# Performance work log

Hardware: AMD Instinct MI355X
Metric: run time of the kernel (lower is better)

## Reference

```python
import jax, jax.numpy as jnp
import numpy as np

D_IN = 2048
D_OUT = 2048
NUM_HEADS = 16
HEAD_DIM = D_OUT // NUM_HEADS  # 128
LATENT_DIM = 256
B, S = 2, 2048


def setup_inputs() -> dict:
    key = jax.random.key(0)
    ks = jax.random.split(key, 7)
    scale = 0.02
    return {
        "x": jax.random.normal(ks[0], (B, S, D_IN), dtype=jnp.float32),
        "W_query": jax.random.normal(ks[1], (D_IN, D_OUT), dtype=jnp.float32) * scale,
        "W_DKV": jax.random.normal(ks[2], (D_IN, LATENT_DIM), dtype=jnp.float32) * scale,
        "W_UKV": jax.random.normal(ks[3], (LATENT_DIM, 2 * D_OUT), dtype=jnp.float32) * scale,
        "W_out": jax.random.normal(ks[4], (D_OUT, D_IN), dtype=jnp.float32) * scale,
        "b_out": jax.random.normal(ks[5], (D_IN,), dtype=jnp.float32) * scale,
        "offset": 0,
    }


def reference(x, W_query, W_DKV, W_UKV, W_out, b_out, offset):
    Bq, Sq, _ = x.shape
    # projections
    q = x @ W_query                      # [B, S, d_out]
    latent = x @ W_DKV                   # [B, S, latent_dim]
    kv = latent @ W_UKV                  # [B, S, 2*d_out]
    k, v = jnp.split(kv, 2, axis=-1)     # each [B, S, d_out]

    def to_heads(t):
        return t.reshape(Bq, Sq, NUM_HEADS, HEAD_DIM).transpose(0, 2, 1, 3)  # [B, H, S, hd]

    qh, kh, vh = to_heads(q), to_heads(k), to_heads(v)

    scores = jnp.einsum("bhqd,bhkd->bhqk", qh, kh)  # [B, H, S, S]
    causal = jnp.tril(jnp.ones((Sq, Sq), dtype=bool))  # True = keep (kv_cache=None -> Sq==Skv)
    # faithful to original: masked_fill(-inf) BEFORE the rsqrt(head_dim) scaling
    scores = jnp.where(causal, scores, -jnp.inf)
    inv_sqrt_d = jax.lax.rsqrt(jnp.asarray(HEAD_DIM, dtype=scores.dtype))
    attn = jax.nn.softmax(scores * inv_sqrt_d, axis=-1)  # dropout p=0 -> identity

    ctx = jnp.einsum("bhqk,bhkd->bhqd", attn, vh)        # [B, H, S, hd]
    ctx = ctx.transpose(0, 2, 1, 3).reshape(Bq, Sq, D_OUT)
    return ctx @ W_out + b_out           # [B, S, d_in]
```

## Files before the change

kernel.cpp:

```cpp
#include <hip/hip_runtime.h>
#include <hip/hip_bf16.h>

typedef short bf16x8 __attribute__((ext_vector_type(8)));
typedef float f32x4 __attribute__((ext_vector_type(4)));
typedef float f32x16 __attribute__((ext_vector_type(16)));
typedef unsigned int u32x4 __attribute__((ext_vector_type(4)));
typedef unsigned short u16;
typedef unsigned short u16x4 __attribute__((ext_vector_type(4)));
typedef unsigned short u16x8 __attribute__((ext_vector_type(8)));

constexpr int D_IN = 2048, D_OUT = 2048, NH = 16, HD = 128, LAT = 256;
constexpr int Bb = 2, Ss = 2048, Mtot = Bb * Ss;

constexpr float QSCALE = 0.08838834764831845f * 1.4426950408889634f;
constexpr float NEG_BIG = -3.0e38f;

__device__ __forceinline__ u16 f2bf(float f) {
  unsigned u = __float_as_uint(f);
  unsigned r = ((u >> 16) & 1u) + 0x7fffu;
  return (u16)((u + r) >> 16);
}

__device__ __forceinline__ float bf2f(u16 v) {
  return __uint_as_float((unsigned)v << 16);
}

__device__ __forceinline__ float fexp2(float x) {
#if __has_builtin(__builtin_amdgcn_exp2f)
  return __builtin_amdgcn_exp2f(x);
#else
  return exp2f(x);
#endif
}

__device__ __forceinline__ unsigned cvtpk(float lo, float hi) {
  unsigned r;
  asm("v_cvt_pk_bf16_f32 %0, %1, %2" : "=v"(r) : "v"(lo), "v"(hi));
  return r;
}

__device__ __forceinline__ void swap32(unsigned& a, unsigned& b) {
  asm volatile("v_permlane32_swap_b32 %0, %1" : "+v"(a), "+v"(b));
}

__device__ __forceinline__ void gload_lds16(const u16* g, u16* l) {
  __builtin_amdgcn_global_load_lds((const __attribute__((address_space(1))) void*)g,
                                   (__attribute__((address_space(3))) void*)l, 16, 0, 0);
}

__global__ void k_cvt_all(const float* __restrict__ x, u16* __restrict__ xb,
                          const float* __restrict__ w0, u16* __restrict__ o0,
                          const float* __restrict__ w1, u16* __restrict__ o1,
                          const float* __restrict__ w2, u16* __restrict__ o2,
                          const float* __restrict__ w3, u16* __restrict__ o3) {
  int id = blockIdx.x;
  const int tx = threadIdx.x, ty = threadIdx.y;
  if (id < 8192) {
    const int i = id * 1024 + (ty * 32 + tx) * 4;
    float4 v = *reinterpret_cast<const float4*>(x + i);
    ushort4 o;
    o.x = f2bf(v.x); o.y = f2bf(v.y); o.z = f2bf(v.z); o.w = f2bf(v.w);
    *reinterpret_cast<ushort4*>(xb + i) = o;
    return;
  }
  id -= 8192;
  __shared__ float t[32][33];
  const float* in;
  u16* out;
  int K, N, bx, by;
  if (id < 4096)      { in = w0; out = o0; K = 2048; N = 2048; bx = (id & 63) * 32; by = (id >> 6) * 32; }
  else if (id < 4608) { id -= 4096; in = w1; out = o1; K = 2048; N = 256;  bx = (id & 7) * 32;  by = (id >> 3) * 32; }
  else if (id < 5632) { id -= 4608; in = w2; out = o2; K = 256;  N = 4096; bx = (id & 127) * 32; by = (id >> 7) * 32; }
  else                { id -= 5632; in = w3; out = o3; K = 2048; N = 2048; bx = (id & 63) * 32; by = (id >> 6) * 32; }
#pragma unroll
  for (int j = 0; j < 32; j += 8)
    t[ty + j][tx] = in[(size_t)(by + ty + j) * N + bx + tx];
  __syncthreads();
#pragma unroll
  for (int j = 0; j < 32; j += 8)
    out[(size_t)(bx + ty + j) * K + by + tx] = f2bf(t[tx][ty + j]);
}

template <int OUT_MODE>
__global__ __launch_bounds__(256) void k_gemm(const u16* __restrict__ A,
                                              const u16* __restrict__ Bt,
                                              void* __restrict__ Cp,
                                              void* __restrict__ Cp2,
                                              const float* __restrict__ bias,
                                              float scale, int M, int N, int K) {
  constexpr int BK = 64;
  __shared__ __align__(16) u16 As[128 * BK];
  __shared__ __align__(16) u16 Bs[128 * BK];
  const int nwg = gridDim.x;
  int bid = blockIdx.x;
  bid = (bid & 7) * (nwg >> 3) + (bid >> 3);
  const int nbx = N >> 7;
  const int bx = bid % nbx, by = bid / nbx;
  const int row0 = by << 7, col0 = bx << 7;
  const int tid = threadIdx.x;
  const int wave = tid >> 6, lane = tid & 63;
  const int wr = (wave >> 1) * 64, wc = (wave & 1) * 64;
  const int lr = lane & 15, lg = lane >> 4;

  f32x4 acc[4][4];
#pragma unroll
  for (int m = 0; m < 4; ++m)
#pragma unroll
    for (int n = 0; n < 4; ++n) acc[m][n] = (f32x4)0.0f;

  const int srow = wave * 32 + (lane >> 3);
  const int scol = ((lane & 7) ^ (lane >> 3)) * 8;
  const u16* gA = A + (size_t)(row0 + srow) * K + scol;
  const u16* gB = Bt + (size_t)(col0 + srow) * K + scol;
  const size_t rstep = (size_t)8 * K;
  u16* lA = &As[(wave * 32) * BK];
  u16* lB = &Bs[(wave * 32) * BK];

  const int rsw = (lr & 7) * 8;

  for (int k0 = 0; k0 < K; k0 += BK) {
#pragma unroll
    for (int c = 0; c < 4; ++c) {
      gload_lds16(gA + c * rstep + k0, lA + c * 8 * BK);
      gload_lds16(gB + c * rstep + k0, lB + c * 8 * BK);
    }
    __syncthreads();
#pragma unroll
    for (int sub = 0; sub < 2; ++sub) {
      const int co = (sub * 32 + lg * 8) ^ rsw;
      bf16x8 af[4], bfr[4];
#pragma unroll
      for (int m = 0; m < 4; ++m)
        af[m] = *reinterpret_cast<const bf16x8*>(&As[(wr + m * 16 + lr) * BK + co]);
#pragma unroll
      for (int n = 0; n < 4; ++n)
        bfr[n] = *reinterpret_cast<const bf16x8*>(&Bs[(wc + n * 16 + lr) * BK + co]);
#pragma unroll
      for (int m = 0; m < 4; ++m)
#pragma unroll
        for (int n = 0; n < 4; ++n)
          acc[m][n] = __builtin_amdgcn_mfma_f32_16x16x32_bf16(af[m], bfr[n], acc[m][n], 0, 0, 0);
    }
    __syncthreads();
  }

#pragma unroll
  for (int m = 0; m < 4; ++m) {
    const int r = row0 + wr + m * 16 + lg * 4;
#pragma unroll
    for (int n = 0; n < 4; ++n) {
      const int c = col0 + wc + n * 16 + lr;
#pragma unroll
      for (int i = 0; i < 4; ++i) {
        float v = acc[m][n][i];
        if (OUT_MODE == 0)
          ((u16*)Cp)[(size_t)(r + i) * N + c] = f2bf(v);
        else if (OUT_MODE == 1)
          ((float*)Cp)[(size_t)(r + i) * N + c] = v + bias[c];
        else {
          if (c < 2048)
            ((u16*)Cp)[(size_t)(r + i) * 2048 + c] = f2bf(v * scale);
          else
            ((u16*)Cp2)[(size_t)(r + i) * 256 + (c - 2048)] = f2bf(v);
        }
      }
    }
  }
}

__device__ __constant__ const signed char S_qb[16] = {7,0, 7,0, 6,0, 6,1, 5,0, 5,2, 4,0, 4,3};
__device__ __constant__ const signed char S_k0[16] = {0,0, 9,0, 0,0, 9,0, 0,0, 9,0, 0,0, 9,0};
__device__ __constant__ const signed char S_k1[16] = {9,0, 16,2, 9,0, 14,4, 9,0, 12,6, 9,0, 10,8};
__device__ __constant__ const signed char S_pm[16] = {0,0, 1,-1, 0,0, 1,-1, 0,0, 1,-1, 0,0, 1,-1};

__global__ __launch_bounds__(512) void k_attn(const u16* __restrict__ Q,
                                              const u16* __restrict__ KV,
                                              u16* __restrict__ O,
                                              u16* __restrict__ o_part,
                                              float* __restrict__ lbuf) {
  __shared__ __align__(16) u16 Ks[128 * 128];
  __shared__ __align__(16) u16 Vt[128 * 128];
  const int job = blockIdx.x >> 5, bh = blockIdx.x & 31;
  const int b = bh >> 4, h = bh & 15;
  const u16* Qb = Q + (size_t)b * Ss * D_OUT + h * HD;
  const u16* Kb = KV + (size_t)b * Ss * (2 * D_OUT) + h * HD;
  const u16* Vb = Kb + D_OUT;
  u16* Ob = O + (size_t)b * Ss * D_OUT + h * HD;

  const int tid = threadIdx.x, wave = tid >> 6, lane = tid & 63;
  const int lo = lane & 31, hi = lane >> 5;

  const int sr = tid >> 2, sc = tid & 3;
  const int vk = (tid & 31) * 4, vd = (tid >> 5) * 8;
  const size_t kvstep = (size_t)128 * 2 * D_OUT;
  const int ksw = (sr & 7) ^ (((sr >> 3) & 3) << 1);
  const int krd = ((lo & 7) * 8) ^ (((lo >> 3) & 3) << 4);

  for (int seg = 0; seg < 2; ++seg) {
    const int kt1 = S_k1[job * 2 + seg];
    if (kt1 == 0) break;
    const int qb = S_qb[job * 2 + seg];
    const int kt0 = S_k0[job * 2 + seg];
    const int pm = S_pm[job * 2 + seg];
    const int q0w = qb * 256 + wave * 32;

    bf16x8 qf[8];
    {
      const u16* qsrc = Qb + (size_t)(q0w + lo) * D_OUT + hi * 8;
#pragma unroll
      for (int ds = 0; ds < 8; ++ds)
        qf[ds] = *reinterpret_cast<const bf16x8*>(qsrc + ds * 16);
    }

    f32x16 ctx[4];
#pragma unroll
    for (int dt = 0; dt < 4; ++dt) ctx[dt] = (f32x16)0.0f;
    float lrow = 0.0f;

    const u16* kg = Kb + (size_t)kt0 * kvstep + (size_t)sr * (2 * D_OUT) + sc * 8;
    const u16* vg = Vb + (size_t)kt0 * kvstep + (size_t)vk * (2 * D_OUT) + vd;

    int4 kreg[4];
    u16x8 vreg[4];
#pragma unroll
    for (int c = 0; c < 4; ++c) {
      kreg[c] = *reinterpret_cast<const int4*>(kg + c * 32);
      vreg[c] = *reinterpret_cast<const u16x8*>(vg + (size_t)c * (2 * D_OUT));
    }

    for (int kt = kt0; kt < kt1; ++kt) {
#pragma unroll
      for (int c = 0; c < 4; ++c)
        *reinterpret_cast<int4*>(&Ks[sr * 128 + (((sc + 4 * c) ^ ksw) * 8)]) = kreg[c];
#pragma unroll
      for (int jj = 0; jj < 8; ++jj) {
        const int vcol = (vk ^ (jj * 8)) ^ ((((vd + jj) >> 3) & 3) << 4);
        u16x4 pk = {vreg[0][jj], vreg[1][jj], vreg[2][jj], vreg[3][jj]};
        *reinterpret_cast<u16x4*>(&Vt[(vd + jj) * 128 + vcol]) = pk;
      }
      if (kt + 1 < kt1) {
        const u16* kn = kg + (size_t)(kt + 1 - kt0) * kvstep;
        const u16* vn = vg + (size_t)(kt + 1 - kt0) * kvstep;
#pragma unroll
        for (int c = 0; c < 4; ++c) {
          kreg[c] = *reinterpret_cast<const int4*>(kn + c * 32);
          vreg[c] = *reinterpret_cast<const u16x8*>(vn + (size_t)c * (2 * D_OUT));
        }
      }
      __syncthreads();

#pragma unroll
      for (int sub = 0; sub < 2; ++sub) {
        const int kbs = kt * 128 + sub * 64;
        if (kbs <= q0w + 31) {
          f32x16 s0 = (f32x16)0.0f, s1 = (f32x16)0.0f;
          __builtin_amdgcn_s_setprio(1);
#pragma unroll
          for (int ds = 0; ds < 8; ++ds) {
            const int off = (16 * ds + 8 * hi) ^ krd;
            bf16x8 a0 = *reinterpret_cast<const bf16x8*>(&Ks[(sub * 64 + lo) * 128 + off]);
            bf16x8 a1 = *reinterpret_cast<const bf16x8*>(&Ks[(sub * 64 + 32 + lo) * 128 + off]);
            s0 = __builtin_amdgcn_mfma_f32_32x32x16_bf16(a0, qf[ds], s0, 0, 0, 0);
            s1 = __builtin_amdgcn_mfma_f32_32x32x16_bf16(a1, qf[ds], s1, 0, 0, 0);
          }
          __builtin_amdgcn_s_setprio(0);

          if (kbs + 63 > q0w) {
            const int qg = q0w + lo;
#pragma unroll
            for (int r = 0; r < 16; ++r) {
              const int koff = kbs + (r & 3) + 8 * (r >> 2) + 4 * hi;
              if (koff > qg) s0[r] = NEG_BIG;
              if (koff + 32 > qg) s1[r] = NEG_BIG;
            }
          }

#pragma unroll
          for (int r = 0; r < 16; ++r) s0[r] = fexp2(s0[r]);
#pragma unroll
          for (int r = 0; r < 16; ++r) s1[r] = fexp2(s1[r]);

          bf16x8 pa[4];
#pragma unroll
          for (int g = 0; g < 2; ++g) {
            const f32x16& sg = g ? s1 : s0;
#pragma unroll
            for (int half = 0; half < 2; ++half) {
              const int rb = half * 8;
              unsigned w0 = cvtpk(sg[rb + 0], sg[rb + 1]);
              unsigned w2 = cvtpk(sg[rb + 4], sg[rb + 5]);
              unsigned w1 = cvtpk(sg[rb + 2], sg[rb + 3]);
              unsigned w3 = cvtpk(sg[rb + 6], sg[rb + 7]);
              swap32(w0, w2);
              swap32(w1, w3);
              u32x4 fr = {w0, w1, w2, w3};
              pa[2 * g + half] = __builtin_bit_cast(bf16x8, fr);
            }
          }

          __builtin_amdgcn_s_setprio(1);
#pragma unroll
          for (int dt = 0; dt < 4; ++dt) {
            const int vrow = 32 * dt + lo;
#pragma unroll
            for (int ks = 0; ks < 4; ++ks) {
              const int off = sub * 64 + ((16 * ks + 8 * hi) ^ krd);
              bf16x8 bv = *reinterpret_cast<const bf16x8*>(&Vt[vrow * 128 + off]);
              ctx[dt] = __builtin_amdgcn_mfma_f32_32x32x16_bf16(pa[ks], bv, ctx[dt], 0, 0, 0);
            }
          }
          __builtin_amdgcn_s_setprio(0);

          float sm[16];
#pragma unroll
          for (int r = 0; r < 16; ++r) sm[r] = s0[r] + s1[r];
#pragma unroll
          for (int w = 8; w >= 1; w >>= 1)
#pragma unroll
            for (int r = 0; r < w; ++r) sm[r] += sm[r + w];
          lrow += sm[0] + __shfl_xor(sm[0], 32);
        }
      }
      __syncthreads();
    }

    if (pm < 0) {
      float linv = 1.0f / lrow;
#pragma unroll
      for (int r = 0; r < 16; ++r) {
        float lb = __shfl(linv, ((r & 3) + 8 * (r >> 2)) + 4 * hi);
        const int qr = q0w + (r & 3) + 8 * (r >> 2) + 4 * hi;
#pragma unroll
        for (int dt = 0; dt < 4; ++dt)
          Ob[(size_t)qr * D_OUT + dt * 32 + lo] = f2bf(ctx[dt][r] * lb);
      }
    } else {
      const int pi = bh * 8 + (qb - 4) * 2 + pm;
      u16* po = o_part + (size_t)pi * (256 * 128);
      float* pl = lbuf + (size_t)pi * 256;
#pragma unroll
      for (int r = 0; r < 16; ++r) {
        const int rl = wave * 32 + (r & 3) + 8 * (r >> 2) + 4 * hi;
#pragma unroll
        for (int dt = 0; dt < 4; ++dt)
          po[rl * 128 + dt * 32 + lo] = f2bf(ctx[dt][r]);
      }
      if (hi == 0) pl[wave * 32 + lo] = lrow;
    }
    __syncthreads();
  }
}

__global__ __launch_bounds__(256) void k_comb(const u16* __restrict__ o_part,
                                              const float* __restrict__ lbuf,
                                              u16* __restrict__ O) {
  const int sb = blockIdx.x >> 2;
  const int rg = blockIdx.x & 3;
  const int bh = sb >> 2, js = sb & 3, qb = 4 + js;
  const int b = bh >> 4, h = bh & 15;
  u16* Ob = O + (size_t)b * Ss * D_OUT + h * HD;
  const int base = bh * 8 + js * 2;
  const u16* po0 = o_part + (size_t)base * (256 * 128);
  const u16* po1 = po0 + 256 * 128;
  const float* pl0 = lbuf + (size_t)base * 256;
  const float* pl1 = pl0 + 256;
  const int tid = threadIdx.x;
  const int r0 = tid >> 4, dg = (tid & 15) * 8;
#pragma unroll
  for (int rp = 0; rp < 4; ++rp) {
    const int row = rg * 64 + rp * 16 + r0;
    const float inv = 1.0f / (pl0[row] + pl1[row]);
    u16x8 o1 = *reinterpret_cast<const u16x8*>(po0 + row * 128 + dg);
    u16x8 o2 = *reinterpret_cast<const u16x8*>(po1 + row * 128 + dg);
    u16x8 o;
#pragma unroll
    for (int j = 0; j < 8; ++j)
      o[j] = f2bf((bf2f(o1[j]) + bf2f(o2[j])) * inv);
    *reinterpret_cast<u16x8*>(&Ob[(size_t)(qb * 256 + row) * D_OUT + dg]) = o;
  }
}

extern "C" void kernel_launch(void* const* d_in, const int* in_sizes, int n_in,
                              void* d_out, int out_size, void* d_ws, size_t ws_size,
                              hipStream_t stream) {
  const float* x    = (const float*)d_in[0];
  const float* Wq   = (const float*)d_in[1];
  const float* Wdkv = (const float*)d_in[2];
  const float* Wukv = (const float*)d_in[3];
  const float* Wout = (const float*)d_in[4];
  const float* bout = (const float*)d_in[5];
  float* out = (float*)d_out;

  char* ws = (char*)d_ws;
  size_t off = 0;
  auto alloc = [&](size_t bytes) -> void* {
    void* p = ws + off;
    off += (bytes + 255) & ~(size_t)255;
    return p;
  };
  u16* xb    = (u16*)alloc((size_t)Mtot * D_IN * 2);
  u16* wcat  = (u16*)alloc((size_t)(D_OUT + LAT) * D_IN * 2);
  u16* wukvT = (u16*)alloc((size_t)2 * D_OUT * LAT * 2);
  u16* woutT = (u16*)alloc((size_t)D_IN * D_OUT * 2);
  u16* q     = (u16*)alloc((size_t)Mtot * D_OUT * 2);
  u16* lat   = (u16*)alloc((size_t)Mtot * LAT * 2);
  u16* kv    = (u16*)alloc((size_t)Mtot * 2 * D_OUT * 2);
  u16* ctx   = (u16*)alloc((size_t)Mtot * D_OUT * 2);
  u16* opart = (u16*)alloc((size_t)256 * 256 * 128 * 2);
  float* lbp = (float*)alloc((size_t)256 * 256 * 4);

  k_cvt_all<<<dim3(8192 + 9728), dim3(32, 8), 0, stream>>>(
      x, xb, Wq, wcat, Wdkv, wcat + (size_t)D_OUT * D_IN, Wukv, wukvT, Wout, woutT);

  k_gemm<3><<<(Mtot / 128) * ((D_OUT + LAT) / 128), 256, 0, stream>>>(
      xb, wcat, q, lat, nullptr, QSCALE, Mtot, D_OUT + LAT, D_IN);
  k_gemm<0><<<(Mtot / 128) * (2 * D_OUT / 128), 256, 0, stream>>>(
      lat, wukvT, kv, nullptr, nullptr, 1.0f, Mtot, 2 * D_OUT, LAT);
  k_attn<<<dim3(8 * 32), 512, 0, stream>>>(q, kv, ctx, opart, lbp);
  k_comb<<<dim3(512), 256, 0, stream>>>(opart, lbp, ctx);
  k_gemm<1><<<(Mtot / 128) * (D_IN / 128), 256, 0, stream>>>(
      ctx, woutT, out, nullptr, bout, 1.0f, Mtot, D_IN, D_OUT);
}
```

Baseline: 197.9 us.

## Rebalance causal attention into 16 jobs per head with multi-way split-KV combine

Replaces the 8-job causal attention schedule with a 16-job-per-(batch,head) schedule in which each job covers about 4-5 KV tiles. Query blocks 1-7 are split into 2-4 partial segments, and the combine kernel now sums a variable number of partials per query block. The aim is to double the number of attention workgroups and even out per-block work so the GPU's compute units stay busy and the long causal tail shrinks. The cost is more partial-output traffic to global memory, a heavier combine pass, and a larger workspace.

Result: slower. 215.0 us (+8.6%).

```diff
diff --git a/kernel.cpp b/kernel.cpp
--- a/kernel.cpp
+++ b/kernel.cpp
@@ -168,10 +168,18 @@
   }
 }
 
-__device__ __constant__ const signed char S_qb[16] = {7,0, 7,0, 6,0, 6,1, 5,0, 5,2, 4,0, 4,3};
-__device__ __constant__ const signed char S_k0[16] = {0,0, 9,0, 0,0, 9,0, 0,0, 9,0, 0,0, 9,0};
-__device__ __constant__ const signed char S_k1[16] = {9,0, 16,2, 9,0, 14,4, 9,0, 12,6, 9,0, 10,8};
-__device__ __constant__ const signed char S_pm[16] = {0,0, 1,-1, 0,0, 1,-1, 0,0, 1,-1, 0,0, 1,-1};
+__device__ __constant__ const signed char S_qb[32] = {
+  7,0, 7,0, 7,0, 7,6, 6,0, 6,0, 5,0, 5,0,
+  5,4, 4,0, 4,0, 3,0, 3,0, 2,0, 2,1, 1,0};
+__device__ __constant__ const signed char S_k0[32] = {
+  0,0, 5,0, 10,0, 15,0, 4,0, 9,0, 0,0, 5,0,
+  10,0, 2,0, 6,0, 0,0, 4,0, 0,0, 4,0, 2,0};
+__device__ __constant__ const signed char S_k1[32] = {
+  5,0, 10,0, 15,0, 16,4, 9,0, 14,0, 5,0, 10,0,
+  12,2, 6,0, 10,0, 4,0, 8,0, 4,0, 6,2, 4,2};
+__device__ __constant__ const signed char S_sl[32] = {
+  15,0, 16,0, 17,0, 18,12, 13,0, 14,0, 9,0, 10,0,
+  11,6, 7,0, 8,0, 4,0, 5,0, 2,0, 3,0, 1,-1};
 
 __global__ __launch_bounds__(512) void k_attn(const u16* __restrict__ Q,
                                               const u16* __restrict__ KV,
@@ -201,7 +209,7 @@
     if (kt1 == 0) break;
     const int qb = S_qb[job * 2 + seg];
     const int kt0 = S_k0[job * 2 + seg];
-    const int pm = S_pm[job * 2 + seg];
+    const int sl = S_sl[job * 2 + seg];
     const int q0w = qb * 256 + wave * 32;
 
     bf16x8 qf[8];
@@ -324,7 +332,7 @@
       __syncthreads();
     }
 
-    if (pm < 0) {
+    if (sl < 0) {
       float linv = 1.0f / lrow;
 #pragma unroll
       for (int r = 0; r < 16; ++r) {
@@ -335,7 +343,7 @@
           Ob[(size_t)qr * D_OUT + dt * 32 + lo] = f2bf(ctx[dt][r] * lb);
       }
     } else {
-      const int pi = bh * 8 + (qb - 4) * 2 + pm;
+      const int pi = bh * 19 + sl;
       u16* po = o_part + (size_t)pi * (256 * 128);
       float* pl = lbuf + (size_t)pi * 256;
 #pragma unroll
@@ -350,32 +358,41 @@
     __syncthreads();
   }
 }
+
+__device__ __constant__ const signed char C_np[7]   = {2, 2, 2, 3, 3, 3, 4};
+__device__ __constant__ const signed char C_base[7] = {0, 2, 4, 6, 9, 12, 15};
 
 __global__ __launch_bounds__(256) void k_comb(const u16* __restrict__ o_part,
                                               const float* __restrict__ lbuf,
                                               u16* __restrict__ O) {
   const int sb = blockIdx.x >> 2;
   const int rg = blockIdx.x & 3;
-  const int bh = sb >> 2, js = sb & 3, qb = 4 + js;
+  const int bh = sb / 7, js = sb % 7, qb = js + 1;
+  const int np = C_np[js];
   const int b = bh >> 4, h = bh & 15;
   u16* Ob = O + (size_t)b * Ss * D_OUT + h * HD;
-  const int base = bh * 8 + js * 2;
-  const u16* po0 = o_part + (size_t)base * (256 * 128);
-  const u16* po1 = po0 + 256 * 128;
-  const float* pl0 = lbuf + (size_t)base * 256;
-  const float* pl1 = pl0 + 256;
+  const int base = bh * 19 + C_base[js];
+  const u16* po = o_part + (size_t)base * (256 * 128);
+  const float* pl = lbuf + (size_t)base * 256;
   const int tid = threadIdx.x;
   const int r0 = tid >> 4, dg = (tid & 15) * 8;
 #pragma unroll
   for (int rp = 0; rp < 4; ++rp) {
     const int row = rg * 64 + rp * 16 + r0;
-    const float inv = 1.0f / (pl0[row] + pl1[row]);
-    u16x8 o1 = *reinterpret_cast<const u16x8*>(po0 + row * 128 + dg);
-    u16x8 o2 = *reinterpret_cast<const u16x8*>(po1 + row * 128 + dg);
+    float lsum = 0.0f;
+    for (int pp = 0; pp < np; ++pp) lsum += pl[pp * 256 + row];
+    const float inv = 1.0f / lsum;
+    float acc[8];
+#pragma unroll
+    for (int j = 0; j < 8; ++j) acc[j] = 0.0f;
+    for (int pp = 0; pp < np; ++pp) {
+      u16x8 ov = *reinterpret_cast<const u16x8*>(po + (size_t)pp * 32768 + row * 128 + dg);
+#pragma unroll
+      for (int j = 0; j < 8; ++j) acc[j] += bf2f(ov[j]);
+    }
     u16x8 o;
 #pragma unroll
-    for (int j = 0; j < 8; ++j)
-      o[j] = f2bf((bf2f(o1[j]) + bf2f(o2[j])) * inv);
+    for (int j = 0; j < 8; ++j) o[j] = f2bf(acc[j] * inv);
     *reinterpret_cast<u16x8*>(&Ob[(size_t)(qb * 256 + row) * D_OUT + dg]) = o;
   }
 }
@@ -406,8 +423,8 @@
   u16* lat   = (u16*)alloc((size_t)Mtot * LAT * 2);
   u16* kv    = (u16*)alloc((size_t)Mtot * 2 * D_OUT * 2);
   u16* ctx   = (u16*)alloc((size_t)Mtot * D_OUT * 2);
-  u16* opart = (u16*)alloc((size_t)256 * 256 * 128 * 2);
-  float* lbp = (float*)alloc((size_t)256 * 256 * 4);
+  u16* opart = (u16*)alloc((size_t)32 * 19 * 256 * 128 * 2);
+  float* lbp = (float*)alloc((size_t)32 * 19 * 256 * 4);
 
   k_cvt_all<<<dim3(8192 + 9728), dim3(32, 8), 0, stream>>>(
       x, xb, Wq, wcat, Wdkv, wcat + (size_t)D_OUT * D_IN, Wukv, wukvT, Wout, woutT);
@@ -416,8 +433,8 @@
       xb, wcat, q, lat, nullptr, QSCALE, Mtot, D_OUT + LAT, D_IN);
   k_gemm<0><<<(Mtot / 128) * (2 * D_OUT / 128), 256, 0, stream>>>(
       lat, wukvT, kv, nullptr, nullptr, 1.0f, Mtot, 2 * D_OUT, LAT);
-  k_attn<<<dim3(8 * 32), 512, 0, stream>>>(q, kv, ctx, opart, lbp);
-  k_comb<<<dim3(512), 256, 0, stream>>>(opart, lbp, ctx);
+  k_attn<<<dim3(16 * 32), 512, 0, stream>>>(q, kv, ctx, opart, lbp);
+  k_comb<<<dim3(896), 256, 0, stream>>>(opart, lbp, ctx);
   k_gemm<1><<<(Mtot / 128) * (D_IN / 128), 256, 0, stream>>>(
       ctx, woutT, out, nullptr, bout, 1.0f, Mtot, D_IN, D_OUT);
 }
```
